# Performance work log

Measured on AMD Instinct MI355X. Metric: run time of the kernel, lower is better.

Reference implementation:

```python
import jax, jax.numpy as jnp
import numpy as np

ADJ_SIZE = 512
START_POS = 128
END_POS = 384
IN_FEATURES = 128
OUT_FEATURES = 128
BATCH = 64
BN_EPS = 1e-5


def setup_inputs() -> dict:
    key = jax.random.key(0)
    k1, k2, k3 = jax.random.split(key, 3)
    inputs = {
        "input": jax.random.normal(k1, (BATCH, ADJ_SIZE, IN_FEATURES), dtype=jnp.float32),
        "adj": jax.random.uniform(k2, (BATCH, ADJ_SIZE, ADJ_SIZE), dtype=jnp.float32),
        "weight": jax.random.normal(k3, (IN_FEATURES, OUT_FEATURES), dtype=jnp.float32) * (1.0 / np.sqrt(IN_FEATURES)),
        "gamma": jnp.ones((OUT_FEATURES * ADJ_SIZE,), dtype=jnp.float32),
        "beta": jnp.zeros((OUT_FEATURES * ADJ_SIZE,), dtype=jnp.float32),
    }
    return inputs


def _crop_mask(n, s, e, dtype):
    # zeros everywhere except the [s:e, s:e] crop block, set to 1
    idx = jnp.arange(n)
    in_crop = (idx >= s) & (idx < e)
    return (in_crop[:, None] & in_crop[None, :]).astype(dtype)  # [N, N]


def reference(input, adj, weight, gamma, beta):
    B, N, _ = input.shape
    # support = input @ weight : [B, N, F_out]
    support = jnp.einsum('bni,io->bno', input, weight)
    # mask adjacency to the crop block
    mask = _crop_mask(N, START_POS, END_POS, adj.dtype)
    adj_ = adj * mask  # [B, N, N]
    # aggregated output : [B, N, F_out]
    output_ = jnp.einsum('bnm,bmf->bnf', adj_, support)
    F = output_.shape[2]
    # BatchNorm1d over flattened (N * F) features, training-mode batch stats
    x = output_.reshape(B, N * F)
    mean = jnp.mean(x, axis=0)
    var = jnp.mean(jnp.square(x - mean), axis=0)  # biased variance (torch BN)
    x_hat = (x - mean) * jax.lax.rsqrt(var + BN_EPS)
    y = x_hat * gamma + beta
    return y.reshape(B, N, F)
```

## Files before the change

kernel.cpp:

```cpp
#include <hip/hip_runtime.h>
#include <hip/hip_bf16.h>

#define BATCH 64
#define NADJ  512
#define F     128
#define CROP0 128
#define CROP1 384
#define CN    256
#define BN_EPS 1e-5f

typedef __attribute__((ext_vector_type(8))) short short8;
typedef __attribute__((ext_vector_type(4))) float f32x4;

__device__ __forceinline__ ushort f2bf(float x) {
  __hip_bfloat16 h = __float2bfloat16(x);
  return *reinterpret_cast<ushort*>(&h);
}

__device__ __forceinline__ float bf2f(ushort u) {
  const unsigned v = (unsigned)u << 16;
  float f;
  __builtin_memcpy(&f, &v, 4);
  return f;
}

__device__ __forceinline__ short8 cvt8(const float4 a, const float4 b) {
  short8 r;
  r[0] = (short)f2bf(a.x); r[1] = (short)f2bf(a.y);
  r[2] = (short)f2bf(a.z); r[3] = (short)f2bf(a.w);
  r[4] = (short)f2bf(b.x); r[5] = (short)f2bf(b.y);
  r[6] = (short)f2bf(b.z); r[7] = (short)f2bf(b.w);
  return r;
}

__global__ __launch_bounds__(512, 1) void gcn_ka(
    const float* __restrict__ input, const float* __restrict__ adj,
    const float* __restrict__ W, const float* __restrict__ beta,
    float* __restrict__ out, ushort* __restrict__ Ocrop) {
  const int x = blockIdx.x & 7, y = blockIdx.x >> 3;
  const int b  = ((y >> 2) << 3) | x;
  const int qt = y & 3;
  __shared__ ushort xt[128][280];
  __shared__ ushort wt[128][136];
  __shared__ ushort tt[64][136];
  const int tid = threadIdx.x;
  const int l = tid & 63, w = tid >> 6;
  const int lr = l & 15, lg = l >> 4;

  const int n0w = qt * 64 + (w & 3) * 16;
  const int wh  = w >> 2;
  const float* a0 =
      adj + ((size_t)b * NADJ + CROP0 + n0w + lr) * NADJ + CROP0;
  float4 xreg[16];
#pragma unroll
  for (int ks = 0; ks < 8; ++ks) {
    const int k0 = ks * 32 + lg * 8;
    xreg[2 * ks]     = *reinterpret_cast<const float4*>(&a0[k0]);
    xreg[2 * ks + 1] = *reinterpret_cast<const float4*>(&a0[k0 + 4]);
  }

  {
    const int gid = blockIdx.x * 512 + tid;
#pragma unroll
    for (int q = 0; q < 4; ++q) {
      const int g2 = gid + q * 131072;
      const int c4 = (g2 & 31) * 4;
      const int rr = (g2 >> 5) & 255;
      const int bb = g2 >> 13;
      const int n  = rr < 128 ? rr : rr + 256;
      const float4 bv =
          *reinterpret_cast<const float4*>(&beta[(size_t)n * F + c4]);
      *reinterpret_cast<float4*>(&out[((size_t)bb * NADJ + n) * F + c4]) = bv;
    }
  }

  {
    const int i0 = tid & 63;
    const int fq = (tid >> 6) * 16;
#pragma unroll
    for (int ih = 0; ih < 2; ++ih) {
      const int i = i0 + ih * 64;
      const float* wr = &W[(size_t)i * F + fq];
      float4 v[4];
#pragma unroll
      for (int q = 0; q < 4; ++q)
        v[q] = reinterpret_cast<const float4*>(wr)[q];
#pragma unroll
      for (int q = 0; q < 4; ++q) {
        wt[fq + q * 4 + 0][i] = f2bf(v[q].x);
        wt[fq + q * 4 + 1][i] = f2bf(v[q].y);
        wt[fq + q * 4 + 2][i] = f2bf(v[q].z);
        wt[fq + q * 4 + 3][i] = f2bf(v[q].w);
      }
    }
  }

  const float* inb = input + ((size_t)b * NADJ + CROP0) * F;
#pragma unroll
  for (int q = 0; q < 16; ++q) {
    const int idx = tid + q * 512;
    const int m   = idx >> 5;
    const int c4  = (idx & 31) * 4;
    const float4 v =
        *reinterpret_cast<const float4*>(&inb[(size_t)m * F + c4]);
    xt[c4 + 0][m] = f2bf(v.x);
    xt[c4 + 1][m] = f2bf(v.y);
    xt[c4 + 2][m] = f2bf(v.z);
    xt[c4 + 3][m] = f2bf(v.w);
  }

  short8 areg[8];
#pragma unroll
  for (int ks = 0; ks < 8; ++ks)
    areg[ks] = cvt8(xreg[2 * ks], xreg[2 * ks + 1]);

  __syncthreads();

  const int if0 = wh * 64;
  f32x4 accT[4] = {};
#pragma unroll
  for (int ks = 0; ks < 8; ++ks) {
    const int k0 = ks * 32 + lg * 8;
#pragma unroll
    for (int fi = 0; fi < 4; ++fi) {
      const short8 bv =
          *reinterpret_cast<const short8*>(&xt[if0 + fi * 16 + lr][k0]);
      accT[fi] = __builtin_amdgcn_mfma_f32_16x16x32_bf16(areg[ks], bv,
                                                         accT[fi], 0, 0, 0);
    }
  }
  const int nloc = (w & 3) * 16;
#pragma unroll
  for (int fi = 0; fi < 4; ++fi) {
    const int i = if0 + fi * 16 + lr;
#pragma unroll
    for (int r = 0; r < 4; ++r)
      tt[nloc + lg * 4 + r][i] = f2bf(accT[fi][r]);
  }
  __syncthreads();

  const int f0 = wh * 64;
  f32x4 acc[4] = {};
#pragma unroll
  for (int ks = 0; ks < 4; ++ks) {
    const int k0 = ks * 32 + lg * 8;
    const short8 av =
        *reinterpret_cast<const short8*>(&tt[nloc + lr][k0]);
#pragma unroll
    for (int fi = 0; fi < 4; ++fi) {
      const short8 bv =
          *reinterpret_cast<const short8*>(&wt[f0 + fi * 16 + lr][k0]);
      acc[fi] =
          __builtin_amdgcn_mfma_f32_16x16x32_bf16(av, bv, acc[fi], 0, 0, 0);
    }
  }

#pragma unroll
  for (int fi = 0; fi < 4; ++fi) {
    const int f = f0 + fi * 16 + lr;
    const int n = n0w + lg * 4;
#pragma unroll
    for (int r = 0; r < 4; ++r)
      Ocrop[((size_t)b * CN + n + r) * F + f] = f2bf(acc[fi][r]);
  }
}

__global__ __launch_bounds__(256) void gcn_kb(
    const ushort* __restrict__ Ocrop, float* __restrict__ out,
    const float* __restrict__ gamma, const float* __restrict__ beta) {
  __shared__ f32x4 s_l[256], s2_l[256];
  __shared__ f32x4 m_l[32], r_l[32];
  const int tid = threadIdx.x;
  const int qq = tid & 31, bg = tid >> 5;
  const int j  = (blockIdx.x * 32 + qq) * 4;
  const int nl = j >> 7, f = j & 127;
  const int nf = (CROP0 + nl) * F + f;
  const ushort* p = Ocrop + (size_t)j + (size_t)bg * 8 * CN * F;

  f32x4 x[8];
  f32x4 s = {0.f, 0.f, 0.f, 0.f}, s2 = {0.f, 0.f, 0.f, 0.f};
#pragma unroll
  for (int bb = 0; bb < 8; ++bb) {
    const ushort4 u =
        *reinterpret_cast<const ushort4*>(&p[(size_t)bb * CN * F]);
    f32x4 v;
    v[0] = bf2f(u.x); v[1] = bf2f(u.y); v[2] = bf2f(u.z); v[3] = bf2f(u.w);
    x[bb] = v;
    s += v;
    s2 += v * v;
  }
  s_l[tid]  = s;
  s2_l[tid] = s2;
  __syncthreads();
  if (tid < 32) {
    f32x4 ts = {0.f, 0.f, 0.f, 0.f}, ts2 = {0.f, 0.f, 0.f, 0.f};
#pragma unroll
    for (int g = 0; g < 8; ++g) {
      ts += s_l[g * 32 + tid];
      ts2 += s2_l[g * 32 + tid];
    }
    const f32x4 mean = ts * (1.f / BATCH);
    const f32x4 var  = ts2 * (1.f / BATCH) - mean * mean;
    f32x4 rs;
    rs[0] = rsqrtf(var[0] + BN_EPS);
    rs[1] = rsqrtf(var[1] + BN_EPS);
    rs[2] = rsqrtf(var[2] + BN_EPS);
    rs[3] = rsqrtf(var[3] + BN_EPS);
    m_l[tid] = mean;
    r_l[tid] = rs;
  }
  __syncthreads();
  const f32x4 mean = m_l[qq];
  const f32x4 rs   = r_l[qq];
  const float4 gm = *reinterpret_cast<const float4*>(&gamma[nf]);
  const float4 bt = *reinterpret_cast<const float4*>(&beta[nf]);
  f32x4 a, c;
  a[0] = rs[0] * gm.x; a[1] = rs[1] * gm.y;
  a[2] = rs[2] * gm.z; a[3] = rs[3] * gm.w;
  c[0] = bt.x - mean[0] * a[0]; c[1] = bt.y - mean[1] * a[1];
  c[2] = bt.z - mean[2] * a[2]; c[3] = bt.w - mean[3] * a[3];
#pragma unroll
  for (int bb = 0; bb < 8; ++bb) {
    const f32x4 yv = x[bb] * a + c;
    *reinterpret_cast<f32x4*>(
        &out[(size_t)nf + (size_t)(bg * 8 + bb) * NADJ * F]) = yv;
  }
}

extern "C" void kernel_launch(void* const* d_in, const int* in_sizes, int n_in,
                              void* d_out, int out_size, void* d_ws,
                              size_t ws_size, hipStream_t stream) {
  const float* input = (const float*)d_in[0];
  const float* adj   = (const float*)d_in[1];
  const float* W     = (const float*)d_in[2];
  const float* gamma = (const float*)d_in[3];
  const float* beta  = (const float*)d_in[4];
  float* out = (float*)d_out;

  ushort* Ocrop = (ushort*)d_ws;

  gcn_ka<<<256, 512, 0, stream>>>(input, adj, W, beta, out, Ocrop);
  gcn_kb<<<256, 256, 0, stream>>>(Ocrop, out, gamma, beta);
}
```

Measured before the change: 25.00 us.

## Compute support first and pipeline input chunks with adjacency aggregation

Replaces the (adj·input)·W ordering with support = input·W computed chunk by chunk over 64-row slices of the cropped input. A double-buffered LDS stage overlaps the global prefetch of the next input and adjacency slices with the MFMA work on the current one. Aggregation with adj then accumulates directly into registers, removing the large transposed input tile and the intermediate tt stage. Lighter barriers that only wait on LDS replace __syncthreads. The added rounding of support to bf16 before aggregation changes numerics slightly, and the extra barriers and register pressure may limit the overlap.

```diff
diff --git a/kernel.cpp b/kernel.cpp
--- a/kernel.cpp
+++ b/kernel.cpp
@@ -33,6 +33,62 @@
   return r;
 }
 
+__device__ __forceinline__ void bar_lds() {
+  asm volatile("s_waitcnt lgkmcnt(0)" ::: "memory");
+  __builtin_amdgcn_s_barrier();
+  asm volatile("" ::: "memory");
+}
+
+#define IN_PREFETCH(PV, CHUNK)                                              \
+  _Pragma("unroll") for (int q = 0; q < 4; ++q)                             \
+      PV[q] = *reinterpret_cast<const float4*>(                             \
+          &inb[(size_t)((CHUNK) * 64 + ml0 + q * 16) * F + ic4]);
+
+#define ADJ_SLICE(SX, C)                                                    \
+  _Pragma("unroll") for (int t = 0; t < 4; ++t)                             \
+      SX[t] = *reinterpret_cast<const float4*>(                             \
+          &a0[(C) * 64 + (t >> 1) * 32 + lg * 8 + (t & 1) * 4]);
+
+#define AIN_WRITE(BUF, PV)                                                  \
+  _Pragma("unroll") for (int q = 0; q < 4; ++q)                             \
+      *reinterpret_cast<ushort4*>(&ain[BUF][ml0 + q * 16][ic4]) =           \
+          make_ushort4(f2bf(PV[q].x), f2bf(PV[q].y), f2bf(PV[q].z),         \
+                       f2bf(PV[q].w));
+
+#define S_CHUNK(CC)                                                         \
+  {                                                                         \
+    f32x4 sacc[4] = {};                                                     \
+    _Pragma("unroll") for (int ks = 0; ks < 4; ++ks) {                      \
+      const int k0 = ks * 32 + lg * 8;                                      \
+      const short8 av =                                                     \
+          *reinterpret_cast<const short8*>(&ain[(CC) & 1][msub + lr][k0]);  \
+      _Pragma("unroll") for (int fi = 0; fi < 4; ++fi) {                    \
+        const short8 bv =                                                   \
+            *reinterpret_cast<const short8*>(&wt[sf0 + fi * 16 + lr][k0]);  \
+        sacc[fi] = __builtin_amdgcn_mfma_f32_16x16x32_bf16(av, bv,          \
+                                                           sacc[fi], 0, 0,  \
+                                                           0);              \
+      }                                                                     \
+    }                                                                       \
+    _Pragma("unroll") for (int fi = 0; fi < 4; ++fi)                        \
+        *reinterpret_cast<ushort4*>(                                        \
+            &stl[sf0 + fi * 16 + lr][(CC) * 64 + msub + lg * 4]) =          \
+            make_ushort4(f2bf(sacc[fi][0]), f2bf(sacc[fi][1]),              \
+                         f2bf(sacc[fi][2]), f2bf(sacc[fi][3]));             \
+  }
+
+#define AGG_SLICE(SX, C)                                                    \
+  _Pragma("unroll") for (int ks2 = 0; ks2 < 2; ++ks2) {                     \
+    const int k0 = (C) * 64 + ks2 * 32 + lg * 8;                            \
+    const short8 av = cvt8(SX[2 * ks2], SX[2 * ks2 + 1]);                   \
+    _Pragma("unroll") for (int fi = 0; fi < 4; ++fi) {                      \
+      const short8 bv =                                                     \
+          *reinterpret_cast<const short8*>(&stl[wf0 + fi * 16 + lr][k0]);   \
+      acc[fi] = __builtin_amdgcn_mfma_f32_16x16x32_bf16(av, bv, acc[fi],    \
+                                                        0, 0, 0);           \
+    }                                                                       \
+  }
+
 __global__ __launch_bounds__(512, 1) void gcn_ka(
     const float* __restrict__ input, const float* __restrict__ adj,
     const float* __restrict__ W, const float* __restrict__ beta,
@@ -40,125 +96,94 @@
   const int x = blockIdx.x & 7, y = blockIdx.x >> 3;
   const int b  = ((y >> 2) << 3) | x;
   const int qt = y & 3;
-  __shared__ ushort xt[128][280];
   __shared__ ushort wt[128][136];
-  __shared__ ushort tt[64][136];
+  __shared__ ushort ain[2][64][136];
+  __shared__ ushort stl[128][268];
   const int tid = threadIdx.x;
   const int l = tid & 63, w = tid >> 6;
   const int lr = l & 15, lg = l >> 4;
-
-  const int n0w = qt * 64 + (w & 3) * 16;
-  const int wh  = w >> 2;
+  const int n0   = qt * 64 + (w & 3) * 16;
+  const int wf0  = (w >> 2) * 64;
+  const int msub = (w & 3) * 16;
+  const int sf0  = (w >> 2) * 64;
+  const int ml0  = tid >> 5;
+  const int ic4  = (tid & 31) * 4;
+  const float* inb = input + ((size_t)b * NADJ + CROP0) * F;
   const float* a0 =
-      adj + ((size_t)b * NADJ + CROP0 + n0w + lr) * NADJ + CROP0;
-  float4 xreg[16];
-#pragma unroll
-  for (int ks = 0; ks < 8; ++ks) {
-    const int k0 = ks * 32 + lg * 8;
-    xreg[2 * ks]     = *reinterpret_cast<const float4*>(&a0[k0]);
-    xreg[2 * ks + 1] = *reinterpret_cast<const float4*>(&a0[k0 + 4]);
-  }
-
-  {
-    const int gid = blockIdx.x * 512 + tid;
+      adj + ((size_t)b * NADJ + CROP0 + n0 + lr) * NADJ + CROP0;
+
+  const int i0 = tid & 63;
+  const int fq = (tid >> 6) * 16;
+  float4 wv[8];
+#pragma unroll
+  for (int ih = 0; ih < 2; ++ih) {
+    const float* wr = &W[(size_t)(i0 + ih * 64) * F + fq];
+#pragma unroll
+    for (int q = 0; q < 4; ++q)
+      wv[ih * 4 + q] = reinterpret_cast<const float4*>(wr)[q];
+  }
+  float4 pv[4], pv2[4];
+  IN_PREFETCH(pv, 0)
+  IN_PREFETCH(pv2, 1)
+  float4 sA[4], sB[4], sC[4], sD[4];
+  ADJ_SLICE(sA, 0)
+  ADJ_SLICE(sB, 1)
+  float4 btv[4];
+  int bidx[4];
+#pragma unroll
+  for (int q = 0; q < 4; ++q) {
+    const int g2 = blockIdx.x * 512 + tid + q * 131072;
+    const int c4 = (g2 & 31) * 4;
+    const int rr = (g2 >> 5) & 255;
+    const int bb = g2 >> 13;
+    const int n  = rr < 128 ? rr : rr + 256;
+    btv[q]  = *reinterpret_cast<const float4*>(&beta[(size_t)n * F + c4]);
+    bidx[q] = ((bb * NADJ + n) << 7) + c4;
+  }
+
+#pragma unroll
+  for (int ih = 0; ih < 2; ++ih) {
+    const int i = i0 + ih * 64;
 #pragma unroll
     for (int q = 0; q < 4; ++q) {
-      const int g2 = gid + q * 131072;
-      const int c4 = (g2 & 31) * 4;
-      const int rr = (g2 >> 5) & 255;
-      const int bb = g2 >> 13;
-      const int n  = rr < 128 ? rr : rr + 256;
-      const float4 bv =
-          *reinterpret_cast<const float4*>(&beta[(size_t)n * F + c4]);
-      *reinterpret_cast<float4*>(&out[((size_t)bb * NADJ + n) * F + c4]) = bv;
+      wt[fq + q * 4 + 0][i] = f2bf(wv[ih * 4 + q].x);
+      wt[fq + q * 4 + 1][i] = f2bf(wv[ih * 4 + q].y);
+      wt[fq + q * 4 + 2][i] = f2bf(wv[ih * 4 + q].z);
+      wt[fq + q * 4 + 3][i] = f2bf(wv[ih * 4 + q].w);
     }
   }
-
-  {
-    const int i0 = tid & 63;
-    const int fq = (tid >> 6) * 16;
-#pragma unroll
-    for (int ih = 0; ih < 2; ++ih) {
-      const int i = i0 + ih * 64;
-      const float* wr = &W[(size_t)i * F + fq];
-      float4 v[4];
-#pragma unroll
-      for (int q = 0; q < 4; ++q)
-        v[q] = reinterpret_cast<const float4*>(wr)[q];
-#pragma unroll
-      for (int q = 0; q < 4; ++q) {
-        wt[fq + q * 4 + 0][i] = f2bf(v[q].x);
-        wt[fq + q * 4 + 1][i] = f2bf(v[q].y);
-        wt[fq + q * 4 + 2][i] = f2bf(v[q].z);
-        wt[fq + q * 4 + 3][i] = f2bf(v[q].w);
-      }
-    }
-  }
-
-  const float* inb = input + ((size_t)b * NADJ + CROP0) * F;
-#pragma unroll
-  for (int q = 0; q < 16; ++q) {
-    const int idx = tid + q * 512;
-    const int m   = idx >> 5;
-    const int c4  = (idx & 31) * 4;
-    const float4 v =
-        *reinterpret_cast<const float4*>(&inb[(size_t)m * F + c4]);
-    xt[c4 + 0][m] = f2bf(v.x);
-    xt[c4 + 1][m] = f2bf(v.y);
-    xt[c4 + 2][m] = f2bf(v.z);
-    xt[c4 + 3][m] = f2bf(v.w);
-  }
-
-  short8 areg[8];
-#pragma unroll
-  for (int ks = 0; ks < 8; ++ks)
-    areg[ks] = cvt8(xreg[2 * ks], xreg[2 * ks + 1]);
-
-  __syncthreads();
-
-  const int if0 = wh * 64;
-  f32x4 accT[4] = {};
-#pragma unroll
-  for (int ks = 0; ks < 8; ++ks) {
-    const int k0 = ks * 32 + lg * 8;
-#pragma unroll
-    for (int fi = 0; fi < 4; ++fi) {
-      const short8 bv =
-          *reinterpret_cast<const short8*>(&xt[if0 + fi * 16 + lr][k0]);
-      accT[fi] = __builtin_amdgcn_mfma_f32_16x16x32_bf16(areg[ks], bv,
-                                                         accT[fi], 0, 0, 0);
-    }
-  }
-  const int nloc = (w & 3) * 16;
+  AIN_WRITE(0, pv)
+  bar_lds();
+
+#pragma unroll
+  for (int q = 0; q < 4; ++q)
+    *reinterpret_cast<float4*>(&out[(size_t)bidx[q]]) = btv[q];
+
+  f32x4 acc[4] = {};
+  ADJ_SLICE(sC, 2)
+  IN_PREFETCH(pv, 2)
+  S_CHUNK(0)
+  AIN_WRITE(1, pv2)
+  bar_lds();
+  ADJ_SLICE(sD, 3)
+  IN_PREFETCH(pv2, 3)
+  AGG_SLICE(sA, 0)
+  S_CHUNK(1)
+  AIN_WRITE(0, pv)
+  bar_lds();
+  AGG_SLICE(sB, 1)
+  S_CHUNK(2)
+  AIN_WRITE(1, pv2)
+  bar_lds();
+  AGG_SLICE(sC, 2)
+  S_CHUNK(3)
+  bar_lds();
+  AGG_SLICE(sD, 3)
+
 #pragma unroll
   for (int fi = 0; fi < 4; ++fi) {
-    const int i = if0 + fi * 16 + lr;
-#pragma unroll
-    for (int r = 0; r < 4; ++r)
-      tt[nloc + lg * 4 + r][i] = f2bf(accT[fi][r]);
-  }
-  __syncthreads();
-
-  const int f0 = wh * 64;
-  f32x4 acc[4] = {};
-#pragma unroll
-  for (int ks = 0; ks < 4; ++ks) {
-    const int k0 = ks * 32 + lg * 8;
-    const short8 av =
-        *reinterpret_cast<const short8*>(&tt[nloc + lr][k0]);
-#pragma unroll
-    for (int fi = 0; fi < 4; ++fi) {
-      const short8 bv =
-          *reinterpret_cast<const short8*>(&wt[f0 + fi * 16 + lr][k0]);
-      acc[fi] =
-          __builtin_amdgcn_mfma_f32_16x16x32_bf16(av, bv, acc[fi], 0, 0, 0);
-    }
-  }
-
-#pragma unroll
-  for (int fi = 0; fi < 4; ++fi) {
-    const int f = f0 + fi * 16 + lr;
-    const int n = n0w + lg * 4;
+    const int f = wf0 + fi * 16 + lr;
+    const int n = n0 + lg * 4;
 #pragma unroll
     for (int r = 0; r < 4; ++r)
       Ocrop[((size_t)b * CN + n + r) * F + f] = f2bf(acc[fi][r]);
@@ -177,7 +202,7 @@
   const int nf = (CROP0 + nl) * F + f;
   const ushort* p = Ocrop + (size_t)j + (size_t)bg * 8 * CN * F;
 
-  f32x4 x[8];
+  f32x4 xv[8];
   f32x4 s = {0.f, 0.f, 0.f, 0.f}, s2 = {0.f, 0.f, 0.f, 0.f};
 #pragma unroll
   for (int bb = 0; bb < 8; ++bb) {
@@ -185,7 +210,7 @@
         *reinterpret_cast<const ushort4*>(&p[(size_t)bb * CN * F]);
     f32x4 v;
     v[0] = bf2f(u.x); v[1] = bf2f(u.y); v[2] = bf2f(u.z); v[3] = bf2f(u.w);
-    x[bb] = v;
+    xv[bb] = v;
     s += v;
     s2 += v * v;
   }
@@ -221,7 +246,7 @@
   c[2] = bt.z - mean[2] * a[2]; c[3] = bt.w - mean[3] * a[3];
 #pragma unroll
   for (int bb = 0; bb < 8; ++bb) {
-    const f32x4 yv = x[bb] * a + c;
+    const f32x4 yv = xv[bb] * a + c;
     *reinterpret_cast<f32x4*>(
         &out[(size_t)nf + (size_t)(bg * 8 + bb) * NADJ * F]) = yv;
   }
```

After: 22.22 us. -11.1%, faster.
